# Performance work log

Hardware: AMD Instinct MI355X
Metric: run time of the kernel (lower is better)

Reference implementation:

```python
import jax, jax.numpy as jnp
from jax import lax
import numpy as np

B, C, T = 8, 512, 8192
RATIO = 2
K = 12  # filter taps for both up and down FIR


def kaiser_sinc_filter1d(cutoff, half_width, kernel_size):
    # Faithful port of BigVGAN's kaiser_sinc_filter1d (even kernel_size path)
    half_size = kernel_size // 2
    delta_f = 4.0 * half_width
    A = 2.285 * (half_size - 1) * np.pi * delta_f + 7.95
    if A > 50.0:
        beta = 0.1102 * (A - 8.7)
    elif A >= 21.0:
        beta = 0.5842 * (A - 21.0) ** 0.4 + 0.07886 * (A - 21.0)
    else:
        beta = 0.0
    window = np.kaiser(kernel_size, beta)
    time = np.arange(-half_size, half_size) + 0.5  # even kernel
    filt = 2.0 * cutoff * window * np.sinc(2.0 * cutoff * time)
    filt = filt / filt.sum()
    return jnp.asarray(filt, dtype=jnp.float32)


def setup_inputs() -> dict:
    key = jax.random.key(0)
    k1, k2 = jax.random.split(key)
    x = jax.random.normal(k1, (B, C, T), dtype=jnp.float32)
    # Snake per-channel alpha parameter in LOG scale (alpha_logscale=True)
    alpha = 0.1 * jax.random.normal(k2, (C,), dtype=jnp.float32)
    # Fixed anti-aliasing low-pass filters (buffers)
    up_filter = kaiser_sinc_filter1d(cutoff=0.5 / RATIO, half_width=0.6 / RATIO, kernel_size=K)
    down_filter = kaiser_sinc_filter1d(cutoff=0.5 / RATIO, half_width=0.6 / RATIO, kernel_size=K)
    return {"x": x, "alpha": alpha, "up_filter": up_filter, "down_filter": down_filter}


def _forward(x, alpha, up_filter, down_filter):
    Bc, Cc, Tc = x.shape
    dn = ("NCH", "OIH", "NCH")
    # ---- UpSample1d: replicate-pad, grouped conv_transpose (stride=RATIO), crop ----
    pad = K // RATIO - 1                                  # 5
    pad_left = pad * RATIO + (K - RATIO) // 2             # 15
    pad_right = pad * RATIO + (K - RATIO + 1) // 2        # 15
    xp = jnp.pad(x, ((0, 0), (0, 0), (pad, pad)), mode="edge")
    w_up = jnp.broadcast_to(up_filter[None, None, :], (Cc, 1, K))
    # conv_transpose1d(stride=s) == input-dilated conv with flipped kernel, full padding
    y = RATIO * lax.conv_general_dilated(
        xp, jnp.flip(w_up, axis=-1),
        window_strides=(1,), padding=[(K - 1, K - 1)],
        lhs_dilation=(RATIO,), dimension_numbers=dn,
        feature_group_count=Cc)
    y = y[..., pad_left:-pad_right]                       # [B, C, RATIO*T]
    # ---- Snake activation (logscale alpha) ----
    a = jnp.exp(alpha)[None, :, None]
    y = y + (1.0 / (a + 1e-9)) * jnp.square(jnp.sin(a * y))
    # ---- DownSample1d: replicate-pad, grouped strided FIR conv ----
    dpl = K // 2 - 1                                       # 5 (even kernel)
    dpr = K // 2                                           # 6
    yp = jnp.pad(y, ((0, 0), (0, 0), (dpl, dpr)), mode="edge")
    w_dn = jnp.broadcast_to(down_filter[None, None, :], (Cc, 1, K))
    out = lax.conv_general_dilated(
        yp, w_dn,
        window_strides=(RATIO,), padding=[(0, 0)],
        dimension_numbers=dn, feature_group_count=Cc)
    return out                                             # [B, C, T]


def reference(x, alpha, up_filter, down_filter):
    return _forward(x, alpha, up_filter, down_filter)
```

## Files before the change

kernel.cpp:

```cpp
#include <hip/hip_runtime.h>

#define T_LEN 8192
#define C_N   512
#define BLOCK 256
#define OPT   8
#define TCHUNK (BLOCK * OPT)
#define NCHUNK 4
#define INV_2PI 0.15915494309189535f

typedef float f32x2 __attribute__((ext_vector_type(2)));


__global__ __launch_bounds__(BLOCK, 4) void act1d_fused(
    const float* __restrict__ x,
    const float* __restrict__ alpha,
    const float* __restrict__ wup_g,
    const float* __restrict__ wdn_g,
    float* __restrict__ out)
{
    const int bc   = blockIdx.x;
    const int c    = bc & (C_N - 1);
    const int tid  = threadIdx.x;
    const int lane = tid & 63;
    const int s_   = lane >> 1;
    const int par  = lane & 1;
    const int b63  = OPT * (tid - lane + 63);

    const float* __restrict__ xrow = x   + (size_t)bc * T_LEN;
    float*       __restrict__ orow = out + (size_t)bc * T_LEN;

    float xr[16], xt[6];
    {
        const int N = OPT * tid;
        if (N >= 8) {
#pragma unroll
            for (int w = 0; w < 4; ++w) {
                const float4 t4 = *reinterpret_cast<const float4*>(xrow + N - 8 + 4 * w);
                xr[4 * w + 0] = t4.x;
                xr[4 * w + 1] = t4.y;
                xr[4 * w + 2] = t4.z;
                xr[4 * w + 3] = t4.w;
            }
        } else {
#pragma unroll
            for (int u = 0; u < 16; ++u)
                xr[u] = xrow[max(N - 8 + u, 0)];
        }
        const int hb = b63 + 2 + s_ + par;
#pragma unroll
        for (int j = 0; j < 6; ++j)
            xt[j] = xrow[hb + j];
    }

    f32x2 cpair[6], dpair[6];
#pragma unroll
    for (int t = 0; t < 6; ++t) {
        cpair[t] = (f32x2){ wup_g[2 * t + 1] + wup_g[2 * t + 1],
                            wup_g[2 * t]     + wup_g[2 * t] };
        dpair[t] = (f32x2){ wdn_g[2 * t + 1], wdn_g[2 * t] };
    }
    const float a     = __expf(alpha[c]);
    const float inv_a = 1.0f / (a + 1e-9f);
    const float ka    = a * INV_2PI;
    const f32x2 ka2   = (f32x2){ ka, ka };
    const f32x2 inva2 = (f32x2){ inv_a, inv_a };

#pragma unroll
    for (int chunk = 0; chunk < NCHUNK; ++chunk) {
        const int N   = chunk * TCHUNK + OPT * tid;
        const int N63 = chunk * TCHUNK + b63;

        float xrN[16], xtN[6];
        if (chunk < NCHUNK - 1) {
            const float* pn = xrow + (chunk + 1) * TCHUNK + OPT * tid - 8;
#pragma unroll
            for (int w = 0; w < 4; ++w) {
                const float4 t4 = *reinterpret_cast<const float4*>(pn + 4 * w);
                xrN[4 * w + 0] = t4.x;
                xrN[4 * w + 1] = t4.y;
                xrN[4 * w + 2] = t4.z;
                xrN[4 * w + 3] = t4.w;
            }
            const int N63n = N63 + TCHUNK;
            const int hbn  = N63n + 2 + s_ + par;
            if (N63n + 12 < T_LEN) {
#pragma unroll
                for (int j = 0; j < 6; ++j)
                    xtN[j] = xrow[hbn + j];
            } else {
#pragma unroll
                for (int j = 0; j < 6; ++j)
                    xtN[j] = xrow[min(hbn + j, T_LEN - 1)];
            }
        }

        asm volatile("" ::: "memory");
        __builtin_amdgcn_sched_barrier(0);

        f32x2 A[14];
#pragma unroll
        for (int p = 1; p <= 8; ++p)
            A[p] = (f32x2){ 0.0f, 0.0f };
#pragma unroll
        for (int u = 3; u <= 15; ++u) {
            const f32x2 su = (f32x2){ xr[u], xr[u] };
#pragma unroll
            for (int t = 0; t < 6; ++t) {
                const int p = u - 7 + t;
                if (p >= 1 && p <= 8)
                    A[p] = __builtin_elementwise_fma(cpair[t], su, A[p]);
            }
        }

        float yh = 0.0f;
#pragma unroll
        for (int j = 0; j < 6; ++j) {
            const float cj = par ? cpair[5 - j].y : cpair[5 - j].x;
            yh = fmaf(cj, xt[j], yh);
        }
        {
            const float s = __builtin_amdgcn_sinf(ka * yh);
            yh = fmaf(s * s, inv_a, yh);
        }

#pragma unroll
        for (int p = 1; p <= 8; ++p) {
            const f32x2 arg = A[p] * ka2;
            const f32x2 s   = (f32x2){ __builtin_amdgcn_sinf(arg.x),
                                       __builtin_amdgcn_sinf(arg.y) };
            A[p] = __builtin_elementwise_fma(s * s, inva2, A[p]);
        }

        if (N == 0) {
            const float v = A[3].x;
            A[1] = (f32x2){ v, v };
            A[2] = (f32x2){ v, v };
            A[3].y = v;
        }

        const bool is63 = (lane == 63);
#pragma unroll
        for (int p = 1; p <= 5; ++p) {
            const float dx = __shfl_down(A[p].x, 1, 64);
            const float dy = __shfl_down(A[p].y, 1, 64);
            const float gx = __int_as_float(
                __builtin_amdgcn_readlane(__float_as_int(yh), 2 * p));
            const float gy = __int_as_float(
                __builtin_amdgcn_readlane(__float_as_int(yh), 2 * p - 1));
            A[8 + p] = (f32x2){ is63 ? gx : dx, is63 ? gy : dy };
        }

        if (N == T_LEN - OPT) {
            const float h5 = A[11].y;
            A[11] = (f32x2){ h5, h5 };
            A[12] = (f32x2){ h5, h5 };
            A[13] = (f32x2){ h5, h5 };
        }

        float o[OPT];
#pragma unroll
        for (int r = 0; r < OPT; ++r) {
            f32x2 P = dpair[0] * A[r + 1];
#pragma unroll
            for (int j = 1; j < 6; ++j)
                P = __builtin_elementwise_fma(dpair[j], A[r + j + 1], P);
            o[r] = P.x + P.y;
        }

        *reinterpret_cast<float4*>(orow + N)     = make_float4(o[0], o[1], o[2], o[3]);
        *reinterpret_cast<float4*>(orow + N + 4) = make_float4(o[4], o[5], o[6], o[7]);

        if (chunk < NCHUNK - 1) {
#pragma unroll
            for (int u = 0; u < 16; ++u)
                xr[u] = xrN[u];
#pragma unroll
            for (int j = 0; j < 6; ++j)
                xt[j] = xtN[j];
        }
    }
}

extern "C" void kernel_launch(void* const* d_in, const int* in_sizes, int n_in,
                              void* d_out, int out_size, void* d_ws, size_t ws_size,
                              hipStream_t stream)
{
    const float* x     = (const float*)d_in[0];
    const float* alpha = (const float*)d_in[1];
    const float* wup   = (const float*)d_in[2];
    const float* wdn   = (const float*)d_in[3];
    float*       out   = (float*)d_out;

    const int B_N  = out_size / (C_N * T_LEN);
    const int grid = B_N * C_N;

    act1d_fused<<<grid, BLOCK, 0, stream>>>(x, alpha, wup, wdn, out);
}
```

Before: 48.22 us.

## Split each row across two blocks with all loads issued upfront

Each (batch, channel) row is now handled by two blocks instead of one, and each block processes two interleaved chunks (p and p+2). Both chunks' inputs are loaded before any compute starts, replacing the rolling prefetch across four sequential chunks. The grid doubles to 8192 blocks, which adds parallelism and memory-level overlap. In exchange, per-block setup (alpha exp, filter coefficients) is duplicated and each thread holds more live registers.

Measured after the change: 47.39 us (median of 2 runs). No clear change (-1.7%).

```diff
diff --git a/kernel.cpp b/kernel.cpp
--- a/kernel.cpp
+++ b/kernel.cpp
@@ -5,11 +5,96 @@
 #define BLOCK 256
 #define OPT   8
 #define TCHUNK (BLOCK * OPT)
-#define NCHUNK 4
 #define INV_2PI 0.15915494309189535f
 
 typedef float f32x2 __attribute__((ext_vector_type(2)));
 
+
+template<bool LEFT, bool RIGHT>
+__device__ __forceinline__ void compute_store(
+    const float* __restrict__ xr, const float* __restrict__ xt,
+    int N, int lane, int par,
+    float* __restrict__ orow,
+    const f32x2* __restrict__ cpair, const f32x2* __restrict__ dpair,
+    float inv_a, float ka, f32x2 ka2, f32x2 inva2)
+{
+    f32x2 A[14];
+#pragma unroll
+    for (int p = 1; p <= 8; ++p)
+        A[p] = (f32x2){ 0.0f, 0.0f };
+#pragma unroll
+    for (int u = 3; u <= 15; ++u) {
+        const f32x2 su = (f32x2){ xr[u], xr[u] };
+#pragma unroll
+        for (int t = 0; t < 6; ++t) {
+            const int p = u - 7 + t;
+            if (p >= 1 && p <= 8)
+                A[p] = __builtin_elementwise_fma(cpair[t], su, A[p]);
+        }
+    }
+
+    float yh = 0.0f;
+#pragma unroll
+    for (int j = 0; j < 6; ++j) {
+        const float cj = par ? cpair[5 - j].y : cpair[5 - j].x;
+        yh = fmaf(cj, xt[j], yh);
+    }
+    {
+        const float s = __builtin_amdgcn_sinf(ka * yh);
+        yh = fmaf(s * s, inv_a, yh);
+    }
+
+#pragma unroll
+    for (int p = 1; p <= 8; ++p) {
+        const f32x2 arg = A[p] * ka2;
+        const f32x2 s   = (f32x2){ __builtin_amdgcn_sinf(arg.x),
+                                   __builtin_amdgcn_sinf(arg.y) };
+        A[p] = __builtin_elementwise_fma(s * s, inva2, A[p]);
+    }
+
+    if (LEFT) {
+        if (N == 0) {
+            const float v = A[3].x;
+            A[1] = (f32x2){ v, v };
+            A[2] = (f32x2){ v, v };
+            A[3].y = v;
+        }
+    }
+
+    const bool is63 = (lane == 63);
+#pragma unroll
+    for (int p = 1; p <= 5; ++p) {
+        const float dx = __shfl_down(A[p].x, 1, 64);
+        const float dy = __shfl_down(A[p].y, 1, 64);
+        const float gx = __int_as_float(
+            __builtin_amdgcn_readlane(__float_as_int(yh), 2 * p));
+        const float gy = __int_as_float(
+            __builtin_amdgcn_readlane(__float_as_int(yh), 2 * p - 1));
+        A[8 + p] = (f32x2){ is63 ? gx : dx, is63 ? gy : dy };
+    }
+
+    if (RIGHT) {
+        if (N == T_LEN - OPT) {
+            const float h5 = A[11].y;
+            A[11] = (f32x2){ h5, h5 };
+            A[12] = (f32x2){ h5, h5 };
+            A[13] = (f32x2){ h5, h5 };
+        }
+    }
+
+    float o[OPT];
+#pragma unroll
+    for (int r = 0; r < OPT; ++r) {
+        f32x2 P = dpair[0] * A[r + 1];
+#pragma unroll
+        for (int j = 1; j < 6; ++j)
+            P = __builtin_elementwise_fma(dpair[j], A[r + j + 1], P);
+        o[r] = P.x + P.y;
+    }
+
+    *reinterpret_cast<float4*>(orow + N)     = make_float4(o[0], o[1], o[2], o[3]);
+    *reinterpret_cast<float4*>(orow + N + 4) = make_float4(o[4], o[5], o[6], o[7]);
+}
 
 __global__ __launch_bounds__(BLOCK, 4) void act1d_fused(
     const float* __restrict__ x,
@@ -18,7 +103,9 @@
     const float* __restrict__ wdn_g,
     float* __restrict__ out)
 {
-    const int bc   = blockIdx.x;
+    const int bx   = blockIdx.x;
+    const int p    = bx & 1;
+    const int bc   = bx >> 1;
     const int c    = bc & (C_N - 1);
     const int tid  = threadIdx.x;
     const int lane = tid & 63;
@@ -29,28 +116,58 @@
     const float* __restrict__ xrow = x   + (size_t)bc * T_LEN;
     float*       __restrict__ orow = out + (size_t)bc * T_LEN;
 
-    float xr[16], xt[6];
-    {
-        const int N = OPT * tid;
-        if (N >= 8) {
-#pragma unroll
-            for (int w = 0; w < 4; ++w) {
-                const float4 t4 = *reinterpret_cast<const float4*>(xrow + N - 8 + 4 * w);
-                xr[4 * w + 0] = t4.x;
-                xr[4 * w + 1] = t4.y;
-                xr[4 * w + 2] = t4.z;
-                xr[4 * w + 3] = t4.w;
-            }
+    const int NA = p * TCHUNK + OPT * tid;
+    const int NB = NA + 2 * TCHUNK;
+
+    float xrA[16], xtA[6], xrB[16], xtB[6];
+
+    if (NA >= 8) {
+#pragma unroll
+        for (int w = 0; w < 4; ++w) {
+            const float4 t4 = *reinterpret_cast<const float4*>(xrow + NA - 8 + 4 * w);
+            xrA[4 * w + 0] = t4.x;
+            xrA[4 * w + 1] = t4.y;
+            xrA[4 * w + 2] = t4.z;
+            xrA[4 * w + 3] = t4.w;
+        }
+    } else {
+#pragma unroll
+        for (int u = 0; u < 16; ++u)
+            xrA[u] = xrow[max(NA - 8 + u, 0)];
+    }
+    {
+        const int hbA = p * TCHUNK + b63 + 2 + s_ + par;
+#pragma unroll
+        for (int j = 0; j < 6; ++j)
+            xtA[j] = xrow[hbA + j];
+    }
+    {
+        const float* pb = xrow + NB - 8;
+#pragma unroll
+        for (int w = 0; w < 4; ++w) {
+            const float4 t4 = *reinterpret_cast<const float4*>(pb + 4 * w);
+            xrB[4 * w + 0] = t4.x;
+            xrB[4 * w + 1] = t4.y;
+            xrB[4 * w + 2] = t4.z;
+            xrB[4 * w + 3] = t4.w;
+        }
+    }
+    {
+        const int N63B = (p + 2) * TCHUNK + b63;
+        const int hbB  = N63B + 2 + s_ + par;
+        if (N63B + 12 < T_LEN) {
+#pragma unroll
+            for (int j = 0; j < 6; ++j)
+                xtB[j] = xrow[hbB + j];
         } else {
 #pragma unroll
-            for (int u = 0; u < 16; ++u)
-                xr[u] = xrow[max(N - 8 + u, 0)];
-        }
-        const int hb = b63 + 2 + s_ + par;
-#pragma unroll
-        for (int j = 0; j < 6; ++j)
-            xt[j] = xrow[hb + j];
-    }
+            for (int j = 0; j < 6; ++j)
+                xtB[j] = xrow[min(hbB + j, T_LEN - 1)];
+        }
+    }
+
+    asm volatile("" ::: "memory");
+    __builtin_amdgcn_sched_barrier(0);
 
     f32x2 cpair[6], dpair[6];
 #pragma unroll
@@ -65,120 +182,10 @@
     const f32x2 ka2   = (f32x2){ ka, ka };
     const f32x2 inva2 = (f32x2){ inv_a, inv_a };
 
-#pragma unroll
-    for (int chunk = 0; chunk < NCHUNK; ++chunk) {
-        const int N   = chunk * TCHUNK + OPT * tid;
-        const int N63 = chunk * TCHUNK + b63;
-
-        float xrN[16], xtN[6];
-        if (chunk < NCHUNK - 1) {
-            const float* pn = xrow + (chunk + 1) * TCHUNK + OPT * tid - 8;
-#pragma unroll
-            for (int w = 0; w < 4; ++w) {
-                const float4 t4 = *reinterpret_cast<const float4*>(pn + 4 * w);
-                xrN[4 * w + 0] = t4.x;
-                xrN[4 * w + 1] = t4.y;
-                xrN[4 * w + 2] = t4.z;
-                xrN[4 * w + 3] = t4.w;
-            }
-            const int N63n = N63 + TCHUNK;
-            const int hbn  = N63n + 2 + s_ + par;
-            if (N63n + 12 < T_LEN) {
-#pragma unroll
-                for (int j = 0; j < 6; ++j)
-                    xtN[j] = xrow[hbn + j];
-            } else {
-#pragma unroll
-                for (int j = 0; j < 6; ++j)
-                    xtN[j] = xrow[min(hbn + j, T_LEN - 1)];
-            }
-        }
-
-        asm volatile("" ::: "memory");
-        __builtin_amdgcn_sched_barrier(0);
-
-        f32x2 A[14];
-#pragma unroll
-        for (int p = 1; p <= 8; ++p)
-            A[p] = (f32x2){ 0.0f, 0.0f };
-#pragma unroll
-        for (int u = 3; u <= 15; ++u) {
-            const f32x2 su = (f32x2){ xr[u], xr[u] };
-#pragma unroll
-            for (int t = 0; t < 6; ++t) {
-                const int p = u - 7 + t;
-                if (p >= 1 && p <= 8)
-                    A[p] = __builtin_elementwise_fma(cpair[t], su, A[p]);
-            }
-        }
-
-        float yh = 0.0f;
-#pragma unroll
-        for (int j = 0; j < 6; ++j) {
-            const float cj = par ? cpair[5 - j].y : cpair[5 - j].x;
-            yh = fmaf(cj, xt[j], yh);
-        }
-        {
-            const float s = __builtin_amdgcn_sinf(ka * yh);
-            yh = fmaf(s * s, inv_a, yh);
-        }
-
-#pragma unroll
-        for (int p = 1; p <= 8; ++p) {
-            const f32x2 arg = A[p] * ka2;
-            const f32x2 s   = (f32x2){ __builtin_amdgcn_sinf(arg.x),
-                                       __builtin_amdgcn_sinf(arg.y) };
-            A[p] = __builtin_elementwise_fma(s * s, inva2, A[p]);
-        }
-
-        if (N == 0) {
-            const float v = A[3].x;
-            A[1] = (f32x2){ v, v };
-            A[2] = (f32x2){ v, v };
-            A[3].y = v;
-        }
-
-        const bool is63 = (lane == 63);
-#pragma unroll
-        for (int p = 1; p <= 5; ++p) {
-            const float dx = __shfl_down(A[p].x, 1, 64);
-            const float dy = __shfl_down(A[p].y, 1, 64);
-            const float gx = __int_as_float(
-                __builtin_amdgcn_readlane(__float_as_int(yh), 2 * p));
-            const float gy = __int_as_float(
-                __builtin_amdgcn_readlane(__float_as_int(yh), 2 * p - 1));
-            A[8 + p] = (f32x2){ is63 ? gx : dx, is63 ? gy : dy };
-        }
-
-        if (N == T_LEN - OPT) {
-            const float h5 = A[11].y;
-            A[11] = (f32x2){ h5, h5 };
-            A[12] = (f32x2){ h5, h5 };
-            A[13] = (f32x2){ h5, h5 };
-        }
-
-        float o[OPT];
-#pragma unroll
-        for (int r = 0; r < OPT; ++r) {
-            f32x2 P = dpair[0] * A[r + 1];
-#pragma unroll
-            for (int j = 1; j < 6; ++j)
-                P = __builtin_elementwise_fma(dpair[j], A[r + j + 1], P);
-            o[r] = P.x + P.y;
-        }
-
-        *reinterpret_cast<float4*>(orow + N)     = make_float4(o[0], o[1], o[2], o[3]);
-        *reinterpret_cast<float4*>(orow + N + 4) = make_float4(o[4], o[5], o[6], o[7]);
-
-        if (chunk < NCHUNK - 1) {
-#pragma unroll
-            for (int u = 0; u < 16; ++u)
-                xr[u] = xrN[u];
-#pragma unroll
-            for (int j = 0; j < 6; ++j)
-                xt[j] = xtN[j];
-        }
-    }
+    compute_store<true,  false>(xrA, xtA, NA, lane, par, orow,
+                                cpair, dpair, inv_a, ka, ka2, inva2);
+    compute_store<false, true >(xrB, xtB, NB, lane, par, orow,
+                                cpair, dpair, inv_a, ka, ka2, inva2);
 }
 
 extern "C" void kernel_launch(void* const* d_in, const int* in_sizes, int n_in,
@@ -192,7 +199,7 @@
     float*       out   = (float*)d_out;
 
     const int B_N  = out_size / (C_N * T_LEN);
-    const int grid = B_N * C_N;
+    const int grid = B_N * C_N * 2;
 
     act1d_fused<<<grid, BLOCK, 0, stream>>>(x, alpha, wup, wdn, out);
 }
```
